# Performance work log

Measured on AMD Instinct MI355X. Metric: run time of the kernel, lower is better.

## Reference

```python
import jax, jax.numpy as jnp
import numpy as np

N_NODES = 50000
N_EDGES = 800000
D_FEAT = 64
HIDDEN = 64
OUT = 2


def setup_inputs() -> dict:
    key = jax.random.key(0)
    ks = jax.random.split(key, 12)
    s = 1.0 / np.sqrt(D_FEAT)
    h = 1.0 / np.sqrt(HIDDEN)
    return {
        "x": jax.random.normal(ks[0], (N_NODES, D_FEAT), jnp.float32),
        "edge_index": jax.random.randint(ks[1], (2, N_EDGES), 0, N_NODES, jnp.int64),
        # SAGEConv layer 1: lin_l (aggregated neighbors, with bias), lin_r (root, no bias)
        "W1l": jax.random.uniform(ks[2], (D_FEAT, HIDDEN), jnp.float32, -s, s),
        "b1": jnp.zeros((HIDDEN,), jnp.float32),
        "W1r": jax.random.uniform(ks[3], (D_FEAT, HIDDEN), jnp.float32, -s, s),
        # SAGEConv layer 2
        "W2l": jax.random.uniform(ks[4], (HIDDEN, HIDDEN), jnp.float32, -h, h),
        "b2": jnp.zeros((HIDDEN,), jnp.float32),
        "W2r": jax.random.uniform(ks[5], (HIDDEN, HIDDEN), jnp.float32, -h, h),
        # final Linear
        "Wlin": jax.random.uniform(ks[6], (HIDDEN, OUT), jnp.float32, -h, h),
        "blin": jnp.zeros((OUT,), jnp.float32),
    }


def _sage_conv(h, src, dst, n_nodes, Wl, bl, Wr):
    # mean-aggregate source features at target nodes (PyG SAGEConv, aggr='mean')
    msgs = h[src]  # [E, d] gather
    agg = jax.ops.segment_sum(msgs, dst, num_segments=n_nodes)
    cnt = jax.ops.segment_sum(jnp.ones((src.shape[0],), h.dtype), dst, num_segments=n_nodes)
    agg = agg / jnp.maximum(cnt, 1.0)[:, None]
    return agg @ Wl + bl + h @ Wr


def reference(x, edge_index, W1l, b1, W1r, W2l, b2, W2r, Wlin, blin):
    src, dst = edge_index[0], edge_index[1]
    n = x.shape[0]
    h1 = jax.nn.relu(_sage_conv(x, src, dst, n, W1l, b1, W1r))
    h2 = jax.nn.relu(_sage_conv(h1, src, dst, n, W2l, b2, W2r))
    return h2 @ Wlin + blin
```

## Files before the change

kernel.cpp:

```cpp
#include <hip/hip_runtime.h>
#include <hip/hip_fp16.h>

namespace {

constexpr int N = 50000;
constexpr int E = 800000;
constexpr int D = 64;
constexpr int TN = 128;
constexpr int APAD = 132;
constexpr int CAP = 64;
constexpr int NR = 256;
constexpr int RW = 196;
constexpr int CAPR = 3584;
constexpr int EPB = 2048;

using floatx2 = __attribute__((ext_vector_type(2))) float;

__device__ __forceinline__ uint2 pack4h(float a, float b, float c, float d) {
  __half2 lo = __floats2half2_rn(a, b);
  __half2 hi = __floats2half2_rn(c, d);
  uint2 u;
  u.x = *reinterpret_cast<unsigned*>(&lo);
  u.y = *reinterpret_cast<unsigned*>(&hi);
  return u;
}

__device__ __forceinline__ unsigned pack4fp8(float a, float b, float c, float d) {
  int u = __builtin_amdgcn_cvt_pk_fp8_f32(a, b, 0, false);
  u = __builtin_amdgcn_cvt_pk_fp8_f32(c, d, u, true);
  return (unsigned)u;
}
__device__ __forceinline__ float4 unpack4fp8(unsigned u) {
  floatx2 lo = __builtin_amdgcn_cvt_pk_f32_fp8((int)u, false);
  floatx2 hi = __builtin_amdgcn_cvt_pk_f32_fp8((int)u, true);
  return make_float4(lo[0], lo[1], hi[0], hi[1]);
}

__device__ __forceinline__ void gemm_core(float (*a_s)[APAD],
                                          const float* __restrict__ Wl,
                                          const float* __restrict__ Wr,
                                          const float* __restrict__ bias,
                                          unsigned* __restrict__ P,
                                          __half* __restrict__ Q, int n, int base) {
  int tid = threadIdx.x;
  int ng = tid & 15;
  int cg = tid >> 4;

  float acc[8][8];
#pragma unroll
  for (int i = 0; i < 8; ++i)
#pragma unroll
    for (int j = 0; j < 8; ++j) acc[i][j] = (j < 4) ? 0.0f : bias[cg * 4 + (j - 4)];

#pragma unroll 4
  for (int k = 0; k < D; ++k) {
    float4 a0 = *(const float4*)&a_s[k][ng * 4];
    float4 a1 = *(const float4*)&a_s[k][64 + ng * 4];
    float4 w0 = *(const float4*)&Wl[k * D + cg * 4];
    float4 w1 = *(const float4*)&Wr[k * D + cg * 4];
    float av[8] = {a0.x, a0.y, a0.z, a0.w, a1.x, a1.y, a1.z, a1.w};
    float wv[8] = {w0.x, w0.y, w0.z, w0.w, w1.x, w1.y, w1.z, w1.w};
#pragma unroll
    for (int i = 0; i < 8; ++i)
#pragma unroll
      for (int j = 0; j < 8; ++j) acc[i][j] = fmaf(av[i], wv[j], acc[i][j]);
  }

  uint2* Qv = (uint2*)Q;
#pragma unroll
  for (int i = 0; i < 8; ++i) {
    int gn = base + ((i < 4) ? (ng * 4 + i) : (64 + ng * 4 + (i - 4)));
    if (gn < n) {
      P[(size_t)gn * 16 + cg] = pack4fp8(acc[i][0], acc[i][1], acc[i][2], acc[i][3]);
      Qv[(size_t)gn * 16 + cg] = pack4h(acc[i][4], acc[i][5], acc[i][6], acc[i][7]);
    }
  }
}

__device__ __forceinline__ void stage_a_f32(float (*a_s)[APAD],
                                            const float* __restrict__ A, int n, int base) {
  int tid = threadIdx.x;
  const float4* A4 = (const float4*)A;
  for (int i = tid; i < TN * 16; i += 256) {
    int node = i & 127;
    int kq = i >> 7;
    int gn = base + node;
    float4 v = (gn < n) ? A4[(size_t)gn * 16 + kq] : make_float4(0.f, 0.f, 0.f, 0.f);
    a_s[kq * 4 + 0][node] = v.x;
    a_s[kq * 4 + 1][node] = v.y;
    a_s[kq * 4 + 2][node] = v.z;
    a_s[kq * 4 + 3][node] = v.w;
  }
  __syncthreads();
}

__device__ __forceinline__ void stage_a_f16(float (*a_s)[APAD],
                                            const __half* __restrict__ A, int n, int base) {
  int tid = threadIdx.x;
  const uint2* A2 = (const uint2*)A;
  for (int i = tid; i < TN * 16; i += 256) {
    int node = i & 127;
    int kq = i >> 7;
    int gn = base + node;
    uint2 u;
    u.x = 0u; u.y = 0u;
    if (gn < n) u = A2[(size_t)gn * 16 + kq];
    float2 fa = __half22float2(*reinterpret_cast<const __half2*>(&u.x));
    float2 fb = __half22float2(*reinterpret_cast<const __half2*>(&u.y));
    a_s[kq * 4 + 0][node] = fa.x;
    a_s[kq * 4 + 1][node] = fa.y;
    a_s[kq * 4 + 2][node] = fb.x;
    a_s[kq * 4 + 3][node] = fb.y;
  }
  __syncthreads();
}

__device__ __forceinline__ void place_phase1(const int* __restrict__ src,
                                             const int* __restrict__ dst,
                                             int* __restrict__ cursor,
                                             unsigned int* __restrict__ staging,
                                             int nE, int blk) {
  __shared__ int hist[NR];
  __shared__ int hist2[NR];
  __shared__ int rbase[NR];
  int t = threadIdx.x;
  for (int i = t; i < NR; i += 256) { hist[i] = 0; hist2[i] = 0; }
  __syncthreads();

  int e0 = blk * EPB + t * 8;
  int rr[8];
  unsigned dlo[8];
#pragma unroll
  for (int j = 0; j < 8; ++j) {
    int e = e0 + j;
    if (e < nE) {
      unsigned d = (unsigned)dst[e];
      unsigned r = d / RW;
      rr[j] = (int)r;
      dlo[j] = d - r * RW;
      atomicAdd(&hist[r], 1);
    } else {
      rr[j] = -1;
    }
  }
  __syncthreads();
  if (t < NR) rbase[t] = hist[t] ? atomicAdd(&cursor[t], hist[t]) : 0;
  __syncthreads();
#pragma unroll
  for (int j = 0; j < 8; ++j) {
    if (rr[j] >= 0) {
      unsigned s = (unsigned)src[e0 + j];
      int q = atomicAdd(&hist2[rr[j]], 1);
      int off = rbase[rr[j]] + q;
      if (off < CAPR)
        staging[(size_t)rr[j] * CAPR + off] = (s << 8) | dlo[j];
    }
  }
}

__global__ __launch_bounds__(256) void gemm_place_kernel(
    const float* __restrict__ A, const float* __restrict__ Wl,
    const float* __restrict__ Wr, const float* __restrict__ bias,
    unsigned* __restrict__ P, __half* __restrict__ Q, int n, int nGB,
    const int* __restrict__ src, const int* __restrict__ dst,
    int* __restrict__ cursor, unsigned int* __restrict__ staging, int nE) {
  __shared__ float a_s[D][APAD];
  if ((int)blockIdx.x < nGB) {
    stage_a_f32(a_s, A, n, blockIdx.x * TN);
    gemm_core(a_s, Wl, Wr, bias, P, Q, n, blockIdx.x * TN);
  } else {
    place_phase1(src, dst, cursor, staging, nE, (int)blockIdx.x - nGB);
  }
}

__global__ __launch_bounds__(256) void place_phase2(
    const unsigned int* __restrict__ staging, const int* __restrict__ cursor,
    unsigned short* __restrict__ bucket, int* __restrict__ cntg) {
  __shared__ int lcnt[RW];
  int t = threadIdx.x;
  int r = blockIdx.x;
  for (int i = t; i < RW; i += 256) lcnt[i] = 0;
  __syncthreads();

  int M = min(cursor[r], CAPR);
  const unsigned int* st = staging + (size_t)r * CAPR;
  int nbase = r * RW;
  for (int i = t; i < M; i += 256) {
    unsigned v = st[i];
    int nl = (int)(v & 255u);
    unsigned s = v >> 8;
    int p = atomicAdd(&lcnt[nl], 1);
    if (p < CAP) bucket[(size_t)(nbase + nl) * CAP + p] = (unsigned short)s;
  }
  __syncthreads();
  for (int i = t; i < RW; i += 256) {
    int node = nbase + i;
    if (node < N) cntg[node] = lcnt[i];
  }
}

__global__ __launch_bounds__(256) void gemm2_kernel(const __half* __restrict__ A,
                                                    const float* __restrict__ Wl,
                                                    const float* __restrict__ Wr,
                                                    const float* __restrict__ bias,
                                                    unsigned* __restrict__ P,
                                                    __half* __restrict__ Q, int n) {
  __shared__ float a_s[D][APAD];
  stage_a_f16(a_s, A, n, blockIdx.x * TN);
  gemm_core(a_s, Wl, Wr, bias, P, Q, n, blockIdx.x * TN);
}

__device__ __forceinline__ float4 gather_node(const unsigned* __restrict__ Pv,
                                              const uint2* __restrict__ Qv,
                                              const unsigned short* __restrict__ bucket,
                                              const int* __restrict__ cntg,
                                              int node, int r, int c4) {
  int ct = cntg[node];
  float scale = 1.0f / fmaxf((float)ct, 1.0f);
  int c = min(ct, CAP);
  const unsigned short* slots = bucket + (size_t)node * CAP;

  float4 a = make_float4(0.f, 0.f, 0.f, 0.f);
  for (int i0 = r; i0 < c; i0 += 16) {
    int cm = c - 1;
    int s0 = slots[i0];
    int s1 = slots[min(i0 + 4, cm)];
    int s2 = slots[min(i0 + 8, cm)];
    int s3 = slots[min(i0 + 12, cm)];
    unsigned u0 = Pv[(size_t)s0 * 16 + c4];
    unsigned u1 = 0u, u2 = 0u, u3 = 0u;
    if (i0 + 4 < c) u1 = Pv[(size_t)s1 * 16 + c4];
    if (i0 + 8 < c) u2 = Pv[(size_t)s2 * 16 + c4];
    if (i0 + 12 < c) u3 = Pv[(size_t)s3 * 16 + c4];
#pragma unroll
    for (int j = 0; j < 4; ++j) {
      unsigned u = (j == 0) ? u0 : (j == 1) ? u1 : (j == 2) ? u2 : u3;
      float4 f = unpack4fp8(u);
      a.x += f.x; a.y += f.y; a.z += f.z; a.w += f.w;
    }
  }
  a.x += __shfl_xor(a.x, 16, 64); a.y += __shfl_xor(a.y, 16, 64);
  a.z += __shfl_xor(a.z, 16, 64); a.w += __shfl_xor(a.w, 16, 64);
  a.x += __shfl_xor(a.x, 32, 64); a.y += __shfl_xor(a.y, 32, 64);
  a.z += __shfl_xor(a.z, 32, 64); a.w += __shfl_xor(a.w, 32, 64);

  uint2 qv = Qv[(size_t)node * 16 + c4];
  float2 qa = __half22float2(*reinterpret_cast<const __half2*>(&qv.x));
  float2 qb = __half22float2(*reinterpret_cast<const __half2*>(&qv.y));
  float4 h;
  h.x = fmaxf(fmaf(a.x, scale, qa.x), 0.f);
  h.y = fmaxf(fmaf(a.y, scale, qa.y), 0.f);
  h.z = fmaxf(fmaf(a.z, scale, qb.x), 0.f);
  h.w = fmaxf(fmaf(a.w, scale, qb.y), 0.f);
  return h;
}

__global__ __launch_bounds__(256) void gather1_kernel(
    const unsigned* __restrict__ P, const __half* __restrict__ Q,
    const unsigned short* __restrict__ bucket, const int* __restrict__ cntg,
    __half* __restrict__ hout, int n) {
  int tid = threadIdx.x;
  int lane = tid & 63;
  int sub = tid >> 6;
  int node = blockIdx.x * 4 + sub;
  if (node >= n) return;

  int r = lane >> 4;
  int c4 = lane & 15;
  float4 h = gather_node(P, (const uint2*)Q, bucket, cntg, node, r, c4);
  if (r == 0)
    ((uint2*)hout)[(size_t)node * 16 + c4] = pack4h(h.x, h.y, h.z, h.w);
}

__global__ __launch_bounds__(256) void gather_final_kernel(
    const unsigned* __restrict__ P, const __half* __restrict__ Q,
    const unsigned short* __restrict__ bucket, const int* __restrict__ cntg,
    const float* __restrict__ Wlin, const float* __restrict__ blin,
    float* __restrict__ outp, int n) {
  int tid = threadIdx.x;
  int lane = tid & 63;
  int sub = tid >> 6;
  int node = blockIdx.x * 4 + sub;
  if (node >= n) return;

  int r = lane >> 4;
  int c4 = lane & 15;
  float4 h = gather_node(P, (const uint2*)Q, bucket, cntg, node, r, c4);

  const float2* W2 = (const float2*)Wlin;
  float2 w0 = W2[c4 * 4 + 0], w1 = W2[c4 * 4 + 1];
  float2 w2 = W2[c4 * 4 + 2], w3 = W2[c4 * 4 + 3];
  float a0 = h.x * w0.x + h.y * w1.x + h.z * w2.x + h.w * w3.x;
  float a1 = h.x * w0.y + h.y * w1.y + h.z * w2.y + h.w * w3.y;
#pragma unroll
  for (int ofs = 8; ofs > 0; ofs >>= 1) {
    a0 += __shfl_xor(a0, ofs, 64);
    a1 += __shfl_xor(a1, ofs, 64);
  }
  if (lane == 0) {
    outp[(size_t)node * 2 + 0] = a0 + blin[0];
    outp[(size_t)node * 2 + 1] = a1 + blin[1];
  }
}

}

extern "C" void kernel_launch(void* const* d_in, const int* in_sizes, int n_in,
                              void* d_out, int out_size, void* d_ws, size_t ws_size,
                              hipStream_t stream) {
  const float* x    = (const float*)d_in[0];
  const int*   ei   = (const int*)d_in[1];
  const float* W1l  = (const float*)d_in[2];
  const float* b1   = (const float*)d_in[3];
  const float* W1r  = (const float*)d_in[4];
  const float* W2l  = (const float*)d_in[5];
  const float* b2   = (const float*)d_in[6];
  const float* W2r  = (const float*)d_in[7];
  const float* Wlin = (const float*)d_in[8];
  const float* blin = (const float*)d_in[9];
  float* out = (float*)d_out;

  char* ws = (char*)d_ws;
  size_t p = 0;
  unsigned*       P1   = (unsigned*)(ws + p);       p += (size_t)N * D;
  __half*         Q1   = (__half*)(ws + p);         p += (size_t)N * D * 2;
  __half*         hh   = (__half*)(ws + p);         p += (size_t)N * D * 2;
  unsigned*       P2   = (unsigned*)(ws + p);       p += (size_t)N * D;
  __half*         Q2   = (__half*)(ws + p);         p += (size_t)N * D * 2;
  unsigned short* bkt  = (unsigned short*)(ws + p); p += (size_t)N * CAP * 2;
  int*            cntg = (int*)(ws + p);            p += (size_t)((N * 4 + 255) & ~255);
  unsigned int*   stg  = (unsigned int*)(ws + p);   p += (size_t)NR * CAPR * 4;
  int*            cur  = (int*)(ws + p);            p += (size_t)NR * 4;

  const int* src = ei;
  const int* dst = ei + E;

  const int GB = (N + TN - 1) / TN;
  const int PB = (E + EPB - 1) / EPB;

  hipMemsetAsync(cur, 0, (size_t)NR * sizeof(int), stream);

  gemm_place_kernel<<<GB + PB, 256, 0, stream>>>(
      x, W1l, W1r, b1, P1, Q1, N, GB, src, dst, cur, stg, E);

  place_phase2<<<NR, 256, 0, stream>>>(stg, cur, bkt, cntg);

  gather1_kernel<<<(N + 3) / 4, 256, 0, stream>>>(P1, Q1, bkt, cntg, hh, N);

  gemm2_kernel<<<GB, 256, 0, stream>>>(hh, W2l, W2r, b2, P2, Q2, N);

  gather_final_kernel<<<(N + 3) / 4, 256, 0, stream>>>(
      P2, Q2, bkt, cntg, Wlin, blin, out, N);
}
```

Baseline: 112.0 us.

## Widen gather to 8-byte fp8 loads per lane and enlarge place_phase2 blocks

The gather kernels now have each lane load 8 fp8 features (uint2) instead of 4, so a 64-lane wave covers 8 edges per step across 8 column groups instead of 4 edges across 16. Reductions and the final linear projection are adjusted to the new lane mapping. This aims to cut the number of load instructions and raise the useful bytes per memory request in the latency-bound neighbor gather, at the cost of more accumulator registers (a min-blocks hint of 6 is added). place_phase2 also moves from 256 to 1024 threads per block so each bucket region is processed with more parallelism.

```diff
diff --git a/kernel.cpp b/kernel.cpp
--- a/kernel.cpp
+++ b/kernel.cpp
@@ -30,10 +30,10 @@
   u = __builtin_amdgcn_cvt_pk_fp8_f32(c, d, u, true);
   return (unsigned)u;
 }
-__device__ __forceinline__ float4 unpack4fp8(unsigned u) {
+__device__ __forceinline__ void acc4fp8(unsigned u, float* a) {
   floatx2 lo = __builtin_amdgcn_cvt_pk_f32_fp8((int)u, false);
   floatx2 hi = __builtin_amdgcn_cvt_pk_f32_fp8((int)u, true);
-  return make_float4(lo[0], lo[1], hi[0], hi[1]);
+  a[0] += lo[0]; a[1] += lo[1]; a[2] += hi[0]; a[3] += hi[1];
 }
 
 __device__ __forceinline__ void gemm_core(float (*a_s)[APAD],
@@ -173,19 +173,19 @@
   }
 }
 
-__global__ __launch_bounds__(256) void place_phase2(
+__global__ __launch_bounds__(1024) void place_phase2(
     const unsigned int* __restrict__ staging, const int* __restrict__ cursor,
     unsigned short* __restrict__ bucket, int* __restrict__ cntg) {
   __shared__ int lcnt[RW];
   int t = threadIdx.x;
   int r = blockIdx.x;
-  for (int i = t; i < RW; i += 256) lcnt[i] = 0;
+  for (int i = t; i < RW; i += 1024) lcnt[i] = 0;
   __syncthreads();
 
   int M = min(cursor[r], CAPR);
   const unsigned int* st = staging + (size_t)r * CAPR;
   int nbase = r * RW;
-  for (int i = t; i < M; i += 256) {
+  for (int i = t; i < M; i += 1024) {
     unsigned v = st[i];
     int nl = (int)(v & 255u);
     unsigned s = v >> 8;
@@ -193,7 +193,7 @@
     if (p < CAP) bucket[(size_t)(nbase + nl) * CAP + p] = (unsigned short)s;
   }
   __syncthreads();
-  for (int i = t; i < RW; i += 256) {
+  for (int i = t; i < RW; i += 1024) {
     int node = nbase + i;
     if (node < N) cntg[node] = lcnt[i];
   }
@@ -210,52 +210,56 @@
   gemm_core(a_s, Wl, Wr, bias, P, Q, n, blockIdx.x * TN);
 }
 
-__device__ __forceinline__ float4 gather_node(const unsigned* __restrict__ Pv,
-                                              const uint2* __restrict__ Qv,
-                                              const unsigned short* __restrict__ bucket,
-                                              const int* __restrict__ cntg,
-                                              int node, int r, int c4) {
+__device__ __forceinline__ void gather_node8(const uint2* __restrict__ Pv2,
+                                             const uint2* __restrict__ Qv,
+                                             const unsigned short* __restrict__ bucket,
+                                             const int* __restrict__ cntg,
+                                             int node, int r8, int c8, float* h) {
   int ct = cntg[node];
   float scale = 1.0f / fmaxf((float)ct, 1.0f);
   int c = min(ct, CAP);
   const unsigned short* slots = bucket + (size_t)node * CAP;
 
-  float4 a = make_float4(0.f, 0.f, 0.f, 0.f);
-  for (int i0 = r; i0 < c; i0 += 16) {
+  float a[8];
+#pragma unroll
+  for (int j = 0; j < 8; ++j) a[j] = 0.0f;
+
+  for (int i0 = r8; i0 < c; i0 += 32) {
     int cm = c - 1;
     int s0 = slots[i0];
-    int s1 = slots[min(i0 + 4, cm)];
-    int s2 = slots[min(i0 + 8, cm)];
-    int s3 = slots[min(i0 + 12, cm)];
-    unsigned u0 = Pv[(size_t)s0 * 16 + c4];
-    unsigned u1 = 0u, u2 = 0u, u3 = 0u;
-    if (i0 + 4 < c) u1 = Pv[(size_t)s1 * 16 + c4];
-    if (i0 + 8 < c) u2 = Pv[(size_t)s2 * 16 + c4];
-    if (i0 + 12 < c) u3 = Pv[(size_t)s3 * 16 + c4];
-#pragma unroll
-    for (int j = 0; j < 4; ++j) {
-      unsigned u = (j == 0) ? u0 : (j == 1) ? u1 : (j == 2) ? u2 : u3;
-      float4 f = unpack4fp8(u);
-      a.x += f.x; a.y += f.y; a.z += f.z; a.w += f.w;
-    }
-  }
-  a.x += __shfl_xor(a.x, 16, 64); a.y += __shfl_xor(a.y, 16, 64);
-  a.z += __shfl_xor(a.z, 16, 64); a.w += __shfl_xor(a.w, 16, 64);
-  a.x += __shfl_xor(a.x, 32, 64); a.y += __shfl_xor(a.y, 32, 64);
-  a.z += __shfl_xor(a.z, 32, 64); a.w += __shfl_xor(a.w, 32, 64);
-
-  uint2 qv = Qv[(size_t)node * 16 + c4];
-  float2 qa = __half22float2(*reinterpret_cast<const __half2*>(&qv.x));
-  float2 qb = __half22float2(*reinterpret_cast<const __half2*>(&qv.y));
-  float4 h;
-  h.x = fmaxf(fmaf(a.x, scale, qa.x), 0.f);
-  h.y = fmaxf(fmaf(a.y, scale, qa.y), 0.f);
-  h.z = fmaxf(fmaf(a.z, scale, qb.x), 0.f);
-  h.w = fmaxf(fmaf(a.w, scale, qb.y), 0.f);
-  return h;
-}
-
-__global__ __launch_bounds__(256) void gather1_kernel(
+    int s1 = slots[min(i0 + 8, cm)];
+    int s2 = slots[min(i0 + 16, cm)];
+    int s3 = slots[min(i0 + 24, cm)];
+    uint2 z; z.x = 0u; z.y = 0u;
+    uint2 u0 = Pv2[(size_t)s0 * 8 + c8];
+    uint2 u1 = z, u2 = z, u3 = z;
+    if (i0 + 8 < c)  u1 = Pv2[(size_t)s1 * 8 + c8];
+    if (i0 + 16 < c) u2 = Pv2[(size_t)s2 * 8 + c8];
+    if (i0 + 24 < c) u3 = Pv2[(size_t)s3 * 8 + c8];
+    acc4fp8(u0.x, a); acc4fp8(u0.y, a + 4);
+    acc4fp8(u1.x, a); acc4fp8(u1.y, a + 4);
+    acc4fp8(u2.x, a); acc4fp8(u2.y, a + 4);
+    acc4fp8(u3.x, a); acc4fp8(u3.y, a + 4);
+  }
+#pragma unroll
+  for (int j = 0; j < 8; ++j) {
+    a[j] += __shfl_xor(a[j], 8, 64);
+    a[j] += __shfl_xor(a[j], 16, 64);
+    a[j] += __shfl_xor(a[j], 32, 64);
+  }
+
+  uint2 q0 = Qv[(size_t)node * 16 + c8 * 2 + 0];
+  uint2 q1 = Qv[(size_t)node * 16 + c8 * 2 + 1];
+  float2 qa = __half22float2(*reinterpret_cast<const __half2*>(&q0.x));
+  float2 qb = __half22float2(*reinterpret_cast<const __half2*>(&q0.y));
+  float2 qc = __half22float2(*reinterpret_cast<const __half2*>(&q1.x));
+  float2 qd = __half22float2(*reinterpret_cast<const __half2*>(&q1.y));
+  float qv[8] = {qa.x, qa.y, qb.x, qb.y, qc.x, qc.y, qd.x, qd.y};
+#pragma unroll
+  for (int j = 0; j < 8; ++j) h[j] = fmaxf(fmaf(a[j], scale, qv[j]), 0.0f);
+}
+
+__global__ __launch_bounds__(256, 6) void gather1_kernel(
     const unsigned* __restrict__ P, const __half* __restrict__ Q,
     const unsigned short* __restrict__ bucket, const int* __restrict__ cntg,
     __half* __restrict__ hout, int n) {
@@ -265,14 +269,20 @@
   int node = blockIdx.x * 4 + sub;
   if (node >= n) return;
 
-  int r = lane >> 4;
-  int c4 = lane & 15;
-  float4 h = gather_node(P, (const uint2*)Q, bucket, cntg, node, r, c4);
-  if (r == 0)
-    ((uint2*)hout)[(size_t)node * 16 + c4] = pack4h(h.x, h.y, h.z, h.w);
-}
-
-__global__ __launch_bounds__(256) void gather_final_kernel(
+  int r8 = lane >> 3;
+  int c8 = lane & 7;
+  float h[8];
+  gather_node8((const uint2*)P, (const uint2*)Q, bucket, cntg, node, r8, c8, h);
+  if (r8 == 0) {
+    uint4 u;
+    uint2 lo = pack4h(h[0], h[1], h[2], h[3]);
+    uint2 hi = pack4h(h[4], h[5], h[6], h[7]);
+    u.x = lo.x; u.y = lo.y; u.z = hi.x; u.w = hi.y;
+    ((uint4*)hout)[(size_t)node * 8 + c8] = u;
+  }
+}
+
+__global__ __launch_bounds__(256, 6) void gather_final_kernel(
     const unsigned* __restrict__ P, const __half* __restrict__ Q,
     const unsigned short* __restrict__ bucket, const int* __restrict__ cntg,
     const float* __restrict__ Wlin, const float* __restrict__ blin,
@@ -283,17 +293,21 @@
   int node = blockIdx.x * 4 + sub;
   if (node >= n) return;
 
-  int r = lane >> 4;
-  int c4 = lane & 15;
-  float4 h = gather_node(P, (const uint2*)Q, bucket, cntg, node, r, c4);
+  int r8 = lane >> 3;
+  int c8 = lane & 7;
+  float h[8];
+  gather_node8((const uint2*)P, (const uint2*)Q, bucket, cntg, node, r8, c8, h);
 
   const float2* W2 = (const float2*)Wlin;
-  float2 w0 = W2[c4 * 4 + 0], w1 = W2[c4 * 4 + 1];
-  float2 w2 = W2[c4 * 4 + 2], w3 = W2[c4 * 4 + 3];
-  float a0 = h.x * w0.x + h.y * w1.x + h.z * w2.x + h.w * w3.x;
-  float a1 = h.x * w0.y + h.y * w1.y + h.z * w2.y + h.w * w3.y;
-#pragma unroll
-  for (int ofs = 8; ofs > 0; ofs >>= 1) {
+  float a0 = 0.f, a1 = 0.f;
+#pragma unroll
+  for (int j = 0; j < 8; ++j) {
+    float2 w = W2[c8 * 8 + j];
+    a0 = fmaf(h[j], w.x, a0);
+    a1 = fmaf(h[j], w.y, a1);
+  }
+#pragma unroll
+  for (int ofs = 4; ofs > 0; ofs >>= 1) {
     a0 += __shfl_xor(a0, ofs, 64);
     a1 += __shfl_xor(a1, ofs, 64);
   }
@@ -343,7 +357,7 @@
   gemm_place_kernel<<<GB + PB, 256, 0, stream>>>(
       x, W1l, W1r, b1, P1, Q1, N, GB, src, dst, cur, stg, E);
 
-  place_phase2<<<NR, 256, 0, stream>>>(stg, cur, bkt, cntg);
+  place_phase2<<<NR, 1024, 0, stream>>>(stg, cur, bkt, cntg);
 
   gather1_kernel<<<(N + 3) / 4, 256, 0, stream>>>(P1, Q1, bkt, cntg, hh, N);
 
```

After: 108.6 us. -3.0%, faster.
